# Performance work log

Measured on AMD Instinct MI355X. Metric: run time of the kernel, lower is better.

The kernel has to match this reference:

```python
import jax, jax.numpy as jnp
import numpy as np
from jax import lax

V = 100000       # vocab_size / num_words
E = 300          # embedding_size (== num_units, required by compare stage)
M = 300          # num_units / mem_dim
NC = 3           # num_classes
L = 128          # leaves per tree -> N = 2L-1 nodes
N = 2 * L - 1


def build_tree(num_leaves):
    # balanced binary tree, postorder node numbering (children before parent)
    left, right = [], []
    def rec(lo, hi):
        if hi - lo == 1:
            left.append(-1); right.append(-1)
            return len(left) - 1
        mid = (lo + hi) // 2
        l = rec(lo, mid)
        r = rec(mid, hi)
        left.append(l); right.append(r)
        return len(left) - 1
    rec(0, num_leaves)
    return np.asarray(left, np.int32), np.asarray(right, np.int32)


def setup_inputs() -> dict:
    key = jax.random.key(0)
    ks = jax.random.split(key, 20)
    l1, r1 = build_tree(L)
    l2, r2 = build_tree(L)
    s = 0.1  # param scale (stands in for orthogonal init)
    inp = {
        "sent1": jax.random.randint(ks[0], (N,), 0, V),
        "sent2": jax.random.randint(ks[1], (N,), 0, V),
        "left1": jnp.asarray(l1), "right1": jnp.asarray(r1),
        "left2": jnp.asarray(l2), "right2": jnp.asarray(r2),
        "emb": jax.random.normal(ks[2], (V, E), jnp.float32),
        # composer x-projections, gate order: [cx, ix, fx, ox]
        "Wx_i": jax.random.normal(ks[3], (4, M, E), jnp.float32) * s,
        "bx_i": jnp.zeros((4, M), jnp.float32),
        # composer h-projections, gate order: [u, i, lf, rf, o]
        "Wl_i": jax.random.normal(ks[4], (5, M, M), jnp.float32) * s,
        "Wr_i": jax.random.normal(ks[5], (5, M, M), jnp.float32) * s,
        "Wx_c": jax.random.normal(ks[6], (4, M, M), jnp.float32) * s,
        "bx_c": jnp.zeros((4, M), jnp.float32),
        "Wl_c": jax.random.normal(ks[7], (5, M, M), jnp.float32) * s,
        "Wr_c": jax.random.normal(ks[8], (5, M, M), jnp.float32) * s,
        "Wc": jax.random.normal(ks[9], (M, 4 * M), jnp.float32) * 0.01,
        "bc": jnp.zeros((M,), jnp.float32),
        "Wa1": jax.random.normal(ks[10], (M, 4 * M), jnp.float32) * 0.01,
        "ba1": jnp.zeros((M,), jnp.float32),
        "Wa2": jax.random.normal(ks[11], (NC, M), jnp.float32) * 0.01,
        "ba2": jnp.zeros((NC,), jnp.float32),
    }
    return inp


def tree_lstm(xg, left, right, Wl, Wr):
    # xg: [N, 4, M] precomputed x-gate terms (cx, ix, fx, ox)
    # Wl/Wr: [5, M, M] hidden-state gate weights (u, i, lf, rf, o)
    n, _, m = xg.shape
    zero = jnp.zeros((m,), xg.dtype)

    def step(carry, t):
        C, H = carry
        i, l, r = t
        lc = jnp.where(l >= 0, C[jnp.maximum(l, 0)], zero)
        lh = jnp.where(l >= 0, H[jnp.maximum(l, 0)], zero)
        rc = jnp.where(r >= 0, C[jnp.maximum(r, 0)], zero)
        rh = jnp.where(r >= 0, H[jnp.maximum(r, 0)], zero)
        gl = jnp.einsum('gmd,d->gm', Wl, lh)  # [5, M]
        gr = jnp.einsum('gmd,d->gm', Wr, rh)
        x = xg[i]  # [4, M]
        u  = jnp.tanh(x[0] + gl[0] + gr[0])
        ig = jax.nn.sigmoid(x[1] + gl[1] + gr[1])
        lf = jax.nn.sigmoid(x[2] + gl[2] + gr[2])  # fx shared for both forgets (as in source)
        rf = jax.nn.sigmoid(x[2] + gl[3] + gr[3])
        c = ig * u + lf * lc + rf * rc
        o = jax.nn.sigmoid(x[3] + gl[4] + gr[4])
        h = o * jnp.tanh(c)
        return (C.at[i].set(c), H.at[i].set(h)), None

    init = (jnp.zeros((n, m), xg.dtype), jnp.zeros((n, m), xg.dtype))
    (_, H), _ = lax.scan(step, init, (jnp.arange(n), left, right))
    return H  # [N, M] all node hidden states in postorder


def reference(sent1, sent2, left1, right1, left2, right2, emb,
              Wx_i, bx_i, Wl_i, Wr_i, Wx_c, bx_c, Wl_c, Wr_c,
              Wc, bc, Wa1, ba1, Wa2, ba2):
    pad = emb.shape[0] - 1  # num_words - 1

    def encode(sent, left, right):
        # leaves embed their token; internal nodes embed PAD (PAD=True path)
        tok = jnp.where(left < 0, sent, pad)
        x = emb[tok]                                        # [N, E]
        xg = jnp.einsum('nd,gmd->ngm', x, Wx_i) + bx_i      # [N, 4, M]
        return tree_lstm(xg, left, right, Wl_i, Wr_i)

    s1 = encode(sent1, left1, right1)  # [N1, M]
    s2 = encode(sent2, left2, right2)  # [N2, M]

    raw = s1 @ s2.T                                         # [N1, N2]
    beta = jax.nn.softmax(raw, axis=1) @ s2                 # aligned to s1
    alpha = jax.nn.softmax(raw.T, axis=1) @ s1              # aligned to s2

    def compare(s, a, left, right):
        feat = jnp.concatenate([s, a, s - a, s * a], axis=-1)  # [N, 4M]
        h = jax.nn.relu(feat @ Wc.T + bc)                      # [N, M]
        xg = jnp.einsum('nd,gmd->ngm', h, Wx_c) + bx_c
        return tree_lstm(xg, left, right, Wl_c, Wr_c)

    v1 = compare(s1, beta, left1, right1)
    v2 = compare(s2, alpha, left2, right2)

    agg = jnp.concatenate([v1.mean(0), v1.max(0), v2.mean(0), v2.max(0)])  # [4M]
    hidden = jax.nn.relu(agg @ Wa1.T + ba1)
    logits = hidden @ Wa2.T + ba2
    return logits[None, :]  # [1, num_classes]
```

## Files before the change

### kernel.cpp

```cpp
#include <hip/hip_runtime.h>
#include <math.h>

#define NN 255
#define MM 300
#define TC 510
#define NBLK 300
#define CHUNK 16

__device__ __forceinline__ float sigm(float x) { return 1.0f / (1.0f + expf(-x)); }

__device__ __forceinline__ float aload(const float* p) {
  return __hip_atomic_load(p, __ATOMIC_RELAXED, __HIP_MEMORY_SCOPE_AGENT);
}
__device__ __forceinline__ void astore(float* p, float v) {
  __hip_atomic_store(p, v, __ATOMIC_RELAXED, __HIP_MEMORY_SCOPE_AGENT);
}

__device__ __forceinline__ void leaf_gate(const float* __restrict__ xgp, int m, float& c, float& h) {
  float x0 = xgp[m], x1 = xgp[300 + m], x3 = xgp[900 + m];
  float u  = tanhf(x0);
  float ig = sigm(x1);
  c = ig * u;
  h = sigm(x3) * tanhf(c);
}

__device__ __forceinline__ void gsync(unsigned* flags, unsigned phase) {
  asm volatile("s_waitcnt vmcnt(0)" ::: "memory");
  __syncthreads();
  unsigned* gate = flags + NBLK;
  if (blockIdx.x == 0) {
    if (threadIdx.x < 64) {
      for (;;) {
        unsigned mn = phase;
        for (int i = 1 + (int)threadIdx.x; i < NBLK; i += 64)
          mn = min(mn, __hip_atomic_load(&flags[i], __ATOMIC_RELAXED, __HIP_MEMORY_SCOPE_AGENT));
        if (__all(mn >= phase)) break;
        __builtin_amdgcn_s_sleep(2);
      }
      if (threadIdx.x == 0)
        __hip_atomic_store(gate, phase, __ATOMIC_RELAXED, __HIP_MEMORY_SCOPE_AGENT);
    }
  } else {
    if (threadIdx.x == 0) {
      __hip_atomic_store(&flags[blockIdx.x], phase, __ATOMIC_RELAXED, __HIP_MEMORY_SCOPE_AGENT);
      while (__hip_atomic_load(gate, __ATOMIC_RELAXED, __HIP_MEMORY_SCOPE_AGENT) < phase)
        __builtin_amdgcn_s_sleep(2);
    }
  }
  __syncthreads();
}

__global__ __launch_bounds__(512) void k_setup(const int* __restrict__ l1, const int* __restrict__ r1,
                                               const int* __restrict__ l2, const int* __restrict__ r2,
                                               int* __restrict__ lists, int* __restrict__ cnt)
{
  __shared__ int lv[TC];
  __shared__ int cs[16];
  int t = threadIdx.x;
  if (t < TC) lv[t] = 0;
  if (t < 16) cs[t] = 0;
  __syncthreads();
  for (int it = 0; it < 12; ++it) {
    int nv = 0;
    if (t < TC) {
      int tr = t >= NN;
      int i  = t - tr * NN;
      const int* L = tr ? l2 : l1;
      const int* R = tr ? r2 : r1;
      int l = L[i], r = R[i];
      nv = (l < 0) ? 0 : 1 + max(lv[tr * NN + l], lv[tr * NN + r]);
    }
    __syncthreads();
    if (t < TC) lv[t] = nv;
    __syncthreads();
  }
  if (t < TC) {
    int tr = t >= NN;
    int i  = t - tr * NN;
    int v  = min(lv[t], 15);
    int pos = atomicAdd(&cs[v], 1);
    lists[v * 256 + pos] = (tr << 8) | i;
  }
  __syncthreads();
  if (t < 16) cnt[t] = cs[t];
}

__global__ __launch_bounds__(256, 2) void k_tree(
    const int* __restrict__ l1, const int* __restrict__ r1,
    const int* __restrict__ l2, const int* __restrict__ r2,
    const float* __restrict__ Wl, const float* __restrict__ Wr,
    const float* __restrict__ xg,
    float* __restrict__ H, float* __restrict__ C,
    const int* __restrict__ lists, const int* __restrict__ cnt,
    unsigned* __restrict__ bar)
{
  __shared__ float Hs[CHUNK][2][320];
  __shared__ float Cs[CHUNK][4][2];
  __shared__ float Xs[CHUNK][4][4];
  __shared__ int es[CHUNK], lcs[CHUNK], rcs[CHUNK];

  const int tid  = threadIdx.x;
  const int lane = tid & 63;
  const int team = tid >> 6;
  const int mblk = blockIdx.x % 75;
  const int grp  = blockIdx.x / 75;
  const int m    = mblk * 4 + team;

  float wl[5][5], wr[5][5];
  #pragma unroll
  for (int g = 0; g < 5; ++g) {
    #pragma unroll
    for (int j = 0; j < 5; ++j) {
      int d = j * 64 + lane;
      size_t o = ((size_t)g * 300 + m) * 300 + d;
      wl[g][j] = (d < 300) ? Wl[o] : 0.f;
      wr[g][j] = (d < 300) ? Wr[o] : 0.f;
    }
  }

  for (int e = blockIdx.x * 256 + tid; e < TC * 300; e += 256 * NBLK) {
    int gi = e / 300;
    int mm = e - gi * 300;
    int tr = gi >= NN;
    int node = gi - tr * NN;
    if ((tr ? l2 : l1)[node] < 0) {
      float c, h;
      leaf_gate(xg + (size_t)gi * 1200, mm, c, h);
      astore(&C[(size_t)gi * 300 + mm], c);
      astore(&H[(size_t)gi * 300 + mm], h);
    }
  }
  gsync(bar, 1);

  for (int lv = 1; lv <= 7; ++lv) {
    int nodes = cnt[lv];
    int npg = (nodes + 3) >> 2;
    int n0 = grp * npg;
    int n1 = min(nodes, n0 + npg);
    for (int nb = n0; nb < n1; nb += CHUNK) {
      int nch = min(CHUNK, n1 - nb);
      __syncthreads();
      if (tid < nch) {
        int e = lists[lv * 256 + nb + tid];
        int tr = e >> 8, node = e & 255;
        es[tid]  = e;
        lcs[tid] = (tr ? l2 : l1)[node];
        rcs[tid] = (tr ? r2 : r1)[node];
      }
      __syncthreads();
      for (int q = tid; q < nch * 8; q += 256) {
        int ni = q >> 3, tm = (q >> 1) & 3, side = q & 1;
        int tr = es[ni] >> 8;
        int child = side ? rcs[ni] : lcs[ni];
        Cs[ni][tm][side] = aload(&C[(size_t)(tr * NN + child) * 300 + mblk * 4 + tm]);
      }
      for (int q = tid; q < nch * 16; q += 256) {
        int ni = q >> 4, tm = (q >> 2) & 3, g = q & 3;
        int e = es[ni];
        int gi = (e >> 8) * NN + (e & 255);
        Xs[ni][tm][g] = xg[(size_t)gi * 1200 + g * 300 + mblk * 4 + tm];
      }
      for (int idx = tid; idx < nch * 640; idx += 256) {
        int ni   = idx / 640;
        int rem  = idx - ni * 640;
        int side = rem >= 320;
        int d    = rem - side * 320;
        float v = 0.f;
        if (d < 300) {
          int tr    = es[ni] >> 8;
          int child = side ? rcs[ni] : lcs[ni];
          v = aload(&H[(size_t)(tr * NN + child) * 300 + d]);
        }
        Hs[ni][side][d] = v;
      }
      __syncthreads();
      #pragma unroll 2
      for (int ni = 0; ni < nch; ++ni) {
        float p0 = 0.f, p1 = 0.f, p2 = 0.f, p3 = 0.f, p4 = 0.f;
        #pragma unroll
        for (int j = 0; j < 5; ++j) {
          float hl = Hs[ni][0][j * 64 + lane];
          float hr = Hs[ni][1][j * 64 + lane];
          p0 += wl[0][j] * hl + wr[0][j] * hr;
          p1 += wl[1][j] * hl + wr[1][j] * hr;
          p2 += wl[2][j] * hl + wr[2][j] * hr;
          p3 += wl[3][j] * hl + wr[3][j] * hr;
          p4 += wl[4][j] * hl + wr[4][j] * hr;
        }
        #pragma unroll
        for (int off = 32; off; off >>= 1) {
          p0 += __shfl_xor(p0, off);
          p1 += __shfl_xor(p1, off);
          p2 += __shfl_xor(p2, off);
          p3 += __shfl_xor(p3, off);
          p4 += __shfl_xor(p4, off);
        }
        if (lane == 0) {
          int e = es[ni];
          int gi = (e >> 8) * NN + (e & 255);
          float lc = Cs[ni][team][0], rc = Cs[ni][team][1];
          float u  = tanhf(Xs[ni][team][0] + p0);
          float ig = sigm (Xs[ni][team][1] + p1);
          float lf = sigm (Xs[ni][team][2] + p2);
          float rf = sigm (Xs[ni][team][2] + p3);
          float o  = sigm (Xs[ni][team][3] + p4);
          float cc = ig * u + lf * lc + rf * rc;
          astore(&C[(size_t)gi * 300 + m], cc);
          astore(&H[(size_t)gi * 300 + m], o * tanhf(cc));
        }
      }
    }
    if (lv < 7) gsync(bar, 1 + lv);
  }
}

__global__ __launch_bounds__(256) void k_xg(const int* __restrict__ sent1, const int* __restrict__ sent2,
                                            const int* __restrict__ l1, const int* __restrict__ l2,
                                            const float* __restrict__ emb, int pad,
                                            const float* __restrict__ W, const float* __restrict__ bias,
                                            const float* __restrict__ hsrc, float* __restrict__ out)
{
  __shared__ float Z[8][300];
  int tx = threadIdx.x, ty = threadIdx.y;
  int t = ty * 64 + tx;
  int colbase = blockIdx.y * 8;
  for (int c = 0; c < 8; ++c) {
    int gcol = colbase + c;
    if (gcol < TC) {
      if (hsrc) {
        for (int k = t; k < 300; k += 256) Z[c][k] = hsrc[(size_t)gcol * 300 + k];
      } else {
        int tr = gcol >= NN;
        int node = gcol - tr * NN;
        const int* L = tr ? l2 : l1;
        const int* S = tr ? sent2 : sent1;
        int tok = (L[node] < 0) ? S[node] : pad;
        const float* e = emb + (size_t)tok * 300;
        for (int k = t; k < 300; k += 256) Z[c][k] = e[k];
      }
    } else {
      for (int k = t; k < 300; k += 256) Z[c][k] = 0.f;
    }
  }
  __syncthreads();
  int r = blockIdx.x * 64 + tx;
  if (r < 1200) {
    float a0 = 0.f, a1 = 0.f;
    const float* wp = W + (size_t)r * 300;
    for (int k = 0; k < 300; k += 4) {
      float4 wv = *(const float4*)(wp + k);
      float4 z0 = *(const float4*)(&Z[ty][k]);
      float4 z1 = *(const float4*)(&Z[ty + 4][k]);
      a0 += wv.x*z0.x + wv.y*z0.y + wv.z*z0.z + wv.w*z0.w;
      a1 += wv.x*z1.x + wv.y*z1.y + wv.z*z1.z + wv.w*z1.w;
    }
    float b = bias[r];
    int g0 = colbase + ty, g1 = colbase + ty + 4;
    if (g0 < TC) out[(size_t)g0 * 1200 + r] = a0 + b;
    if (g1 < TC) out[(size_t)g1 * 1200 + r] = a1 + b;
  }
}

__global__ __launch_bounds__(256) void k_attn(const float* __restrict__ Henc, float* __restrict__ ab)
{
  __shared__ float q[300];
  __shared__ float pr[NN];
  __shared__ float red[256];
  int b = blockIdx.x, t = threadIdx.x;
  int dir = b >= NN;
  int i = b - dir * NN;
  const float* Ss = Henc + (dir ? NN * 300 : 0);
  const float* So = Henc + (dir ? 0 : NN * 300);
  for (int k = t; k < 300; k += 256) q[k] = Ss[(size_t)i * 300 + k];
  __syncthreads();
  float v = -1e30f;
  if (t < NN) {
    const float* row = So + (size_t)t * 300;
    float a = 0.f;
    for (int k = 0; k < 300; k += 4) {
      float4 rv = *(const float4*)(row + k);
      float4 qv = *(const float4*)(&q[k]);
      a += rv.x*qv.x + rv.y*qv.y + rv.z*qv.z + rv.w*qv.w;
    }
    pr[t] = a;
    v = a;
  }
  red[t] = v;
  __syncthreads();
  for (int s = 128; s > 0; s >>= 1) { if (t < s) red[t] = fmaxf(red[t], red[t + s]); __syncthreads(); }
  float mx = red[0];
  __syncthreads();
  float e = 0.f;
  if (t < NN) { e = expf(pr[t] - mx); pr[t] = e; }
  red[t] = e;
  __syncthreads();
  for (int s = 128; s > 0; s >>= 1) { if (t < s) red[t] += red[t + s]; __syncthreads(); }
  float inv = 1.0f / red[0];
  __syncthreads();
  for (int m = t; m < 300; m += 256) {
    float a = 0.f;
    for (int j = 0; j < NN; ++j) a += pr[j] * So[(size_t)j * 300 + m];
    ab[(size_t)b * 300 + m] = a * inv;
  }
}

__global__ __launch_bounds__(256) void k_hcmp(const float* __restrict__ Henc, const float* __restrict__ ab,
                                              const float* __restrict__ Wc, const float* __restrict__ bc,
                                              float* __restrict__ hc)
{
  __shared__ float Z[8][1200];
  int tx = threadIdx.x, ty = threadIdx.y;
  int t = ty * 64 + tx;
  int colbase = blockIdx.y * 8;
  for (int c = 0; c < 8; ++c) {
    int gcol = colbase + c;
    if (gcol < TC) {
      const float* sp = Henc + (size_t)gcol * 300;
      const float* ap = ab + (size_t)gcol * 300;
      for (int k = t; k < 1200; k += 256) {
        int sel = k >= 900 ? 3 : (k >= 600 ? 2 : (k >= 300 ? 1 : 0));
        int kk = k - sel * 300;
        float s = sp[kk], a = ap[kk];
        Z[c][k] = sel == 0 ? s : sel == 1 ? a : sel == 2 ? (s - a) : (s * a);
      }
    } else {
      for (int k = t; k < 1200; k += 256) Z[c][k] = 0.f;
    }
  }
  __syncthreads();
  int r = blockIdx.x * 64 + tx;
  if (r < 300) {
    float a0 = 0.f, a1 = 0.f;
    const float* wp = Wc + (size_t)r * 1200;
    for (int k = 0; k < 1200; k += 4) {
      float4 wv = *(const float4*)(wp + k);
      float4 z0 = *(const float4*)(&Z[ty][k]);
      float4 z1 = *(const float4*)(&Z[ty + 4][k]);
      a0 += wv.x*z0.x + wv.y*z0.y + wv.z*z0.z + wv.w*z0.w;
      a1 += wv.x*z1.x + wv.y*z1.y + wv.z*z1.z + wv.w*z1.w;
    }
    float b = bc[r];
    int g0 = colbase + ty, g1 = colbase + ty + 4;
    if (g0 < TC) hc[(size_t)g0 * 300 + r] = fmaxf(a0 + b, 0.f);
    if (g1 < TC) hc[(size_t)g1 * 300 + r] = fmaxf(a1 + b, 0.f);
  }
}

__global__ __launch_bounds__(256) void k_agg(const float* __restrict__ Hcmp, float* __restrict__ agg)
{
  int tr = blockIdx.x, t = threadIdx.x;
  for (int m = t; m < 300; m += 256) {
    float s = 0.f, mx = -1e30f;
    const float* hp = Hcmp + (size_t)tr * NN * 300 + m;
    for (int n = 0; n < NN; ++n) { float v = hp[(size_t)n * 300]; s += v; mx = fmaxf(mx, v); }
    agg[tr * 600 + m] = s / 255.0f;
    agg[tr * 600 + 300 + m] = mx;
  }
}

__global__ __launch_bounds__(512) void k_mlp(const float* __restrict__ agg,
                                             const float* __restrict__ Wa1, const float* __restrict__ ba1,
                                             const float* __restrict__ Wa2, const float* __restrict__ ba2,
                                             float* __restrict__ out)
{
  __shared__ float a_s[1200];
  __shared__ float hid[300];
  int t = threadIdx.x;
  for (int k = t; k < 1200; k += 512) a_s[k] = agg[k];
  __syncthreads();
  for (int h = t; h < 300; h += 512) {
    float acc = ba1[h];
    const float* wp = Wa1 + (size_t)h * 1200;
    for (int k = 0; k < 1200; k += 4) {
      float4 wv = *(const float4*)(wp + k);
      float4 av = *(const float4*)(&a_s[k]);
      acc += wv.x*av.x + wv.y*av.y + wv.z*av.z + wv.w*av.w;
    }
    hid[h] = fmaxf(acc, 0.f);
  }
  __syncthreads();
  if (t < 192) {
    int c = t >> 6, lane = t & 63;
    float a = 0.f;
    for (int k = lane; k < 300; k += 64) a += Wa2[c * 300 + k] * hid[k];
    for (int off = 32; off > 0; off >>= 1) a += __shfl_down(a, off);
    if (lane == 0) out[c] = a + ba2[c];
  }
}

extern "C" void kernel_launch(void* const* d_in, const int* in_sizes, int n_in,
                              void* d_out, int out_size, void* d_ws, size_t ws_size,
                              hipStream_t stream)
{
  const int*   sent1 = (const int*)d_in[0];
  const int*   sent2 = (const int*)d_in[1];
  const int*   l1    = (const int*)d_in[2];
  const int*   r1    = (const int*)d_in[3];
  const int*   l2    = (const int*)d_in[4];
  const int*   r2    = (const int*)d_in[5];
  const float* emb   = (const float*)d_in[6];
  const float* Wx_i  = (const float*)d_in[7];
  const float* bx_i  = (const float*)d_in[8];
  const float* Wl_i  = (const float*)d_in[9];
  const float* Wr_i  = (const float*)d_in[10];
  const float* Wx_c  = (const float*)d_in[11];
  const float* bx_c  = (const float*)d_in[12];
  const float* Wl_c  = (const float*)d_in[13];
  const float* Wr_c  = (const float*)d_in[14];
  const float* Wc    = (const float*)d_in[15];
  const float* bc    = (const float*)d_in[16];
  const float* Wa1   = (const float*)d_in[17];
  const float* ba1   = (const float*)d_in[18];
  const float* Wa2   = (const float*)d_in[19];
  const float* ba2   = (const float*)d_in[20];
  int V = in_sizes[6] / 300;
  int pad = V - 1;

  char* w = (char*)d_ws;
  unsigned* bar1 = (unsigned*)w;
  unsigned* bar2 = (unsigned*)(w + 2048);
  int* cnt   = (int*)(w + 4096);
  int* lists = (int*)(w + 4160);
  float* xg   = (float*)(w + 20544);
  float* Henc = xg + 612000;
  float* Hcmp = Henc + 153000;
  float* C    = Hcmp + 153000;
  float* ab   = C + 153000;
  float* hc   = ab + 153000;
  float* agg  = hc + 153000;

  hipMemsetAsync((void*)bar1, 0, 4096, stream);
  k_setup<<<1, 512, 0, stream>>>(l1, r1, l2, r2, lists, cnt);

  dim3 blk(64, 4);

  k_xg<<<dim3(19, 64), blk, 0, stream>>>(sent1, sent2, l1, l2, emb, pad, Wx_i, bx_i, nullptr, xg);
  {
    void* args[] = {(void*)&l1, (void*)&r1, (void*)&l2, (void*)&r2,
                    (void*)&Wl_i, (void*)&Wr_i, (void*)&xg,
                    (void*)&Henc, (void*)&C, (void*)&lists, (void*)&cnt, (void*)&bar1};
    hipLaunchCooperativeKernel((void*)k_tree, dim3(NBLK), dim3(256), args, 0, stream);
  }

  k_attn<<<TC, 256, 0, stream>>>(Henc, ab);

  k_hcmp<<<dim3(5, 64), blk, 0, stream>>>(Henc, ab, Wc, bc, hc);
  k_xg<<<dim3(19, 64), blk, 0, stream>>>(sent1, sent2, l1, l2, emb, pad, Wx_c, bx_c, hc, xg);
  {
    void* args[] = {(void*)&l1, (void*)&r1, (void*)&l2, (void*)&r2,
                    (void*)&Wl_c, (void*)&Wr_c, (void*)&xg,
                    (void*)&Hcmp, (void*)&C, (void*)&lists, (void*)&cnt, (void*)&bar2};
    hipLaunchCooperativeKernel((void*)k_tree, dim3(NBLK), dim3(256), args, 0, stream);
  }

  k_agg<<<2, 256, 0, stream>>>(Hcmp, agg);
  k_mlp<<<1, 512, 0, stream>>>(agg, Wa1, ba1, Wa2, ba2, (float*)d_out);
}
```

Before: 550.7 us.

## Precompute child-index lists, write transposed H, fuse agg into head kernel

The setup kernel now stores each node's global index and both child indices as an int4, and the tree kernel caches these lists in shared memory once. This removes per-chunk lookups into the left/right arrays. The tree kernel also writes a transposed copy of H so the attention dot products and the mean/max aggregation read coalesced columns, and the aggregation is folded into the MLP head to drop one launch. Child H rows are gathered with explicit unrolled per-team loads. The cost is extra scattered transposed stores on the serial critical path, plus more registers in the cooperative kernel.

```diff
diff --git a/kernel.cpp b/kernel.cpp
--- a/kernel.cpp
+++ b/kernel.cpp
@@ -6,6 +6,7 @@
 #define TC 510
 #define NBLK 300
 #define CHUNK 16
+#define HTLD 512
 
 __device__ __forceinline__ float sigm(float x) { return 1.0f / (1.0f + expf(-x)); }
 
@@ -52,7 +53,7 @@
 
 __global__ __launch_bounds__(512) void k_setup(const int* __restrict__ l1, const int* __restrict__ r1,
                                                const int* __restrict__ l2, const int* __restrict__ r2,
-                                               int* __restrict__ lists, int* __restrict__ cnt)
+                                               int4* __restrict__ lists2, int* __restrict__ cnt)
 {
   __shared__ int lv[TC];
   __shared__ int cs[16];
@@ -79,25 +80,26 @@
     int i  = t - tr * NN;
     int v  = min(lv[t], 15);
     int pos = atomicAdd(&cs[v], 1);
-    lists[v * 256 + pos] = (tr << 8) | i;
+    int l = (tr ? l2 : l1)[i], r = (tr ? r2 : r1)[i];
+    lists2[v * 256 + pos] = make_int4(tr * NN + i, tr * NN + max(l, 0), tr * NN + max(r, 0), 0);
   }
   __syncthreads();
   if (t < 16) cnt[t] = cs[t];
 }
 
 __global__ __launch_bounds__(256, 2) void k_tree(
-    const int* __restrict__ l1, const int* __restrict__ r1,
-    const int* __restrict__ l2, const int* __restrict__ r2,
+    const int* __restrict__ l1, const int* __restrict__ l2,
     const float* __restrict__ Wl, const float* __restrict__ Wr,
     const float* __restrict__ xg,
-    float* __restrict__ H, float* __restrict__ C,
-    const int* __restrict__ lists, const int* __restrict__ cnt,
+    float* __restrict__ H, float* __restrict__ C, float* __restrict__ HT,
+    const int4* __restrict__ lists2, const int* __restrict__ cnt,
     unsigned* __restrict__ bar)
 {
   __shared__ float Hs[CHUNK][2][320];
   __shared__ float Cs[CHUNK][4][2];
   __shared__ float Xs[CHUNK][4][4];
-  __shared__ int es[CHUNK], lcs[CHUNK], rcs[CHUNK];
+  __shared__ int4 nfo[288];
+  __shared__ int lvoff[9];
 
   const int tid  = threadIdx.x;
   const int lane = tid & 63;
@@ -117,6 +119,12 @@
       wr[g][j] = (d < 300) ? Wr[o] : 0.f;
     }
   }
+
+  if (tid == 0) { int o = 0; for (int lv = 1; lv <= 7; ++lv) { lvoff[lv] = o; o += cnt[lv]; } }
+  __syncthreads();
+  for (int lv = 1; lv <= 7; ++lv)
+    for (int i = tid; i < cnt[lv]; i += 256)
+      nfo[lvoff[lv] + i] = lists2[lv * 256 + i];
 
   for (int e = blockIdx.x * 256 + tid; e < TC * 300; e += 256 * NBLK) {
     int gi = e / 300;
@@ -128,6 +136,7 @@
       leaf_gate(xg + (size_t)gi * 1200, mm, c, h);
       astore(&C[(size_t)gi * 300 + mm], c);
       astore(&H[(size_t)gi * 300 + mm], h);
+      astore(&HT[(size_t)mm * HTLD + gi], h);
     }
   }
   gsync(bar, 1);
@@ -139,41 +148,62 @@
     int n1 = min(nodes, n0 + npg);
     for (int nb = n0; nb < n1; nb += CHUNK) {
       int nch = min(CHUNK, n1 - nb);
+      int base = lvoff[lv] + nb;
       __syncthreads();
-      if (tid < nch) {
-        int e = lists[lv * 256 + nb + tid];
-        int tr = e >> 8, node = e & 255;
-        es[tid]  = e;
-        lcs[tid] = (tr ? l2 : l1)[node];
-        rcs[tid] = (tr ? r2 : r1)[node];
+
+      #pragma unroll
+      for (int p = 0; p < 2; ++p) {
+        int niA = team + p * 8;
+        int niB = niA + 4;
+        bool vA = niA < nch, vB = niB < nch;
+        int4 na = vA ? nfo[base + niA] : make_int4(0, 0, 0, 0);
+        int4 nb4 = vB ? nfo[base + niB] : make_int4(0, 0, 0, 0);
+        float bA0, bA1, bA2, bA3, bA4, bA5, bA6, bA7, bA8, bA9;
+        float bB0, bB1, bB2, bB3, bB4, bB5, bB6, bB7, bB8, bB9;
+        #define LD(side_ptr, d, ok) ((ok) ? aload(&H[(size_t)(side_ptr) * 300 + (d)]) : 0.f)
+        {
+          int d0 = lane, d1 = 64 + lane, d2 = 128 + lane, d3 = 192 + lane, d4 = 256 + lane;
+          bool i4 = d4 < 300;
+          bA0 = LD(na.y, d0, vA); bA1 = LD(na.y, d1, vA); bA2 = LD(na.y, d2, vA);
+          bA3 = LD(na.y, d3, vA); bA4 = LD(na.y, d4, vA && i4);
+          bA5 = LD(na.z, d0, vA); bA6 = LD(na.z, d1, vA); bA7 = LD(na.z, d2, vA);
+          bA8 = LD(na.z, d3, vA); bA9 = LD(na.z, d4, vA && i4);
+          bB0 = LD(nb4.y, d0, vB); bB1 = LD(nb4.y, d1, vB); bB2 = LD(nb4.y, d2, vB);
+          bB3 = LD(nb4.y, d3, vB); bB4 = LD(nb4.y, d4, vB && i4);
+          bB5 = LD(nb4.z, d0, vB); bB6 = LD(nb4.z, d1, vB); bB7 = LD(nb4.z, d2, vB);
+          bB8 = LD(nb4.z, d3, vB); bB9 = LD(nb4.z, d4, vB && i4);
+          if (vA) {
+            Hs[niA][0][d0] = bA0; Hs[niA][0][d1] = bA1; Hs[niA][0][d2] = bA2;
+            Hs[niA][0][d3] = bA3; Hs[niA][0][d4] = bA4;
+            Hs[niA][1][d0] = bA5; Hs[niA][1][d1] = bA6; Hs[niA][1][d2] = bA7;
+            Hs[niA][1][d3] = bA8; Hs[niA][1][d4] = bA9;
+          }
+          if (vB) {
+            Hs[niB][0][d0] = bB0; Hs[niB][0][d1] = bB1; Hs[niB][0][d2] = bB2;
+            Hs[niB][0][d3] = bB3; Hs[niB][0][d4] = bB4;
+            Hs[niB][1][d0] = bB5; Hs[niB][1][d1] = bB6; Hs[niB][1][d2] = bB7;
+            Hs[niB][1][d3] = bB8; Hs[niB][1][d4] = bB9;
+          }
+        }
+        #undef LD
+      }
+      if (tid < 128) {
+        int ni = tid >> 3, tm = (tid >> 1) & 3, side = tid & 1;
+        if (ni < nch) {
+          int4 nn = nfo[base + ni];
+          int child = side ? nn.z : nn.y;
+          Cs[ni][tm][side] = aload(&C[(size_t)child * 300 + mblk * 4 + tm]);
+        }
+      }
+      {
+        int ni = tid >> 4, tm = (tid >> 2) & 3, g = tid & 3;
+        if (ni < nch) {
+          int4 nn = nfo[base + ni];
+          Xs[ni][tm][g] = xg[(size_t)nn.x * 1200 + g * 300 + mblk * 4 + tm];
+        }
       }
       __syncthreads();
-      for (int q = tid; q < nch * 8; q += 256) {
-        int ni = q >> 3, tm = (q >> 1) & 3, side = q & 1;
-        int tr = es[ni] >> 8;
-        int child = side ? rcs[ni] : lcs[ni];
-        Cs[ni][tm][side] = aload(&C[(size_t)(tr * NN + child) * 300 + mblk * 4 + tm]);
-      }
-      for (int q = tid; q < nch * 16; q += 256) {
-        int ni = q >> 4, tm = (q >> 2) & 3, g = q & 3;
-        int e = es[ni];
-        int gi = (e >> 8) * NN + (e & 255);
-        Xs[ni][tm][g] = xg[(size_t)gi * 1200 + g * 300 + mblk * 4 + tm];
-      }
-      for (int idx = tid; idx < nch * 640; idx += 256) {
-        int ni   = idx / 640;
-        int rem  = idx - ni * 640;
-        int side = rem >= 320;
-        int d    = rem - side * 320;
-        float v = 0.f;
-        if (d < 300) {
-          int tr    = es[ni] >> 8;
-          int child = side ? rcs[ni] : lcs[ni];
-          v = aload(&H[(size_t)(tr * NN + child) * 300 + d]);
-        }
-        Hs[ni][side][d] = v;
-      }
-      __syncthreads();
+
       #pragma unroll 2
       for (int ni = 0; ni < nch; ++ni) {
         float p0 = 0.f, p1 = 0.f, p2 = 0.f, p3 = 0.f, p4 = 0.f;
@@ -196,8 +226,8 @@
           p4 += __shfl_xor(p4, off);
         }
         if (lane == 0) {
-          int e = es[ni];
-          int gi = (e >> 8) * NN + (e & 255);
+          int4 nn = nfo[base + ni];
+          int gi = nn.x;
           float lc = Cs[ni][team][0], rc = Cs[ni][team][1];
           float u  = tanhf(Xs[ni][team][0] + p0);
           float ig = sigm (Xs[ni][team][1] + p1);
@@ -205,8 +235,10 @@
           float rf = sigm (Xs[ni][team][2] + p3);
           float o  = sigm (Xs[ni][team][3] + p4);
           float cc = ig * u + lf * lc + rf * rc;
+          float hv = o * tanhf(cc);
           astore(&C[(size_t)gi * 300 + m], cc);
-          astore(&H[(size_t)gi * 300 + m], o * tanhf(cc));
+          astore(&H[(size_t)gi * 300 + m], hv);
+          astore(&HT[(size_t)m * HTLD + gi], hv);
         }
       }
     }
@@ -261,7 +293,8 @@
   }
 }
 
-__global__ __launch_bounds__(256) void k_attn(const float* __restrict__ Henc, float* __restrict__ ab)
+__global__ __launch_bounds__(256) void k_attn(const float* __restrict__ H, const float* __restrict__ HT,
+                                              float* __restrict__ ab)
 {
   __shared__ float q[300];
   __shared__ float pr[NN];
@@ -269,19 +302,17 @@
   int b = blockIdx.x, t = threadIdx.x;
   int dir = b >= NN;
   int i = b - dir * NN;
-  const float* Ss = Henc + (dir ? NN * 300 : 0);
-  const float* So = Henc + (dir ? 0 : NN * 300);
+  const float* Ss = H + (dir ? NN * 300 : 0);
+  const float* So = H + (dir ? 0 : NN * 300);
+  int oppb = dir ? 0 : NN;
   for (int k = t; k < 300; k += 256) q[k] = Ss[(size_t)i * 300 + k];
   __syncthreads();
   float v = -1e30f;
   if (t < NN) {
-    const float* row = So + (size_t)t * 300;
     float a = 0.f;
-    for (int k = 0; k < 300; k += 4) {
-      float4 rv = *(const float4*)(row + k);
-      float4 qv = *(const float4*)(&q[k]);
-      a += rv.x*qv.x + rv.y*qv.y + rv.z*qv.z + rv.w*qv.w;
-    }
+    const float* hp = HT + oppb + t;
+    #pragma unroll 4
+    for (int k = 0; k < 300; ++k) a += q[k] * hp[(size_t)k * HTLD];
     pr[t] = a;
     v = a;
   }
@@ -346,27 +377,23 @@
   }
 }
 
-__global__ __launch_bounds__(256) void k_agg(const float* __restrict__ Hcmp, float* __restrict__ agg)
-{
-  int tr = blockIdx.x, t = threadIdx.x;
-  for (int m = t; m < 300; m += 256) {
-    float s = 0.f, mx = -1e30f;
-    const float* hp = Hcmp + (size_t)tr * NN * 300 + m;
-    for (int n = 0; n < NN; ++n) { float v = hp[(size_t)n * 300]; s += v; mx = fmaxf(mx, v); }
-    agg[tr * 600 + m] = s / 255.0f;
-    agg[tr * 600 + 300 + m] = mx;
-  }
-}
-
-__global__ __launch_bounds__(512) void k_mlp(const float* __restrict__ agg,
-                                             const float* __restrict__ Wa1, const float* __restrict__ ba1,
-                                             const float* __restrict__ Wa2, const float* __restrict__ ba2,
-                                             float* __restrict__ out)
+__global__ __launch_bounds__(512) void k_head(const float* __restrict__ HTc,
+                                              const float* __restrict__ Wa1, const float* __restrict__ ba1,
+                                              const float* __restrict__ Wa2, const float* __restrict__ ba2,
+                                              float* __restrict__ out)
 {
   __shared__ float a_s[1200];
   __shared__ float hid[300];
   int t = threadIdx.x;
-  for (int k = t; k < 1200; k += 512) a_s[k] = agg[k];
+  for (int idx = t; idx < 600; idx += 512) {
+    int tr = idx >= 300;
+    int m = idx - tr * 300;
+    const float* p = HTc + (size_t)m * HTLD + tr * NN;
+    float s = 0.f, mx = -1e30f;
+    for (int n = 0; n < NN; ++n) { float v = p[n]; s += v; mx = fmaxf(mx, v); }
+    a_s[tr * 600 + m] = s / 255.0f;
+    a_s[tr * 600 + 300 + m] = mx;
+  }
   __syncthreads();
   for (int h = t; h < 300; h += 512) {
     float acc = ba1[h];
@@ -419,40 +446,42 @@
   char* w = (char*)d_ws;
   unsigned* bar1 = (unsigned*)w;
   unsigned* bar2 = (unsigned*)(w + 2048);
-  int* cnt   = (int*)(w + 4096);
-  int* lists = (int*)(w + 4160);
-  float* xg   = (float*)(w + 20544);
+  int* cnt     = (int*)(w + 4096);
+  int4* lists2 = (int4*)(w + 4160);
+  float* xg   = (float*)(w + 4160 + 65536);
   float* Henc = xg + 612000;
   float* Hcmp = Henc + 153000;
   float* C    = Hcmp + 153000;
   float* ab   = C + 153000;
   float* hc   = ab + 153000;
-  float* agg  = hc + 153000;
+  float* HTe  = hc + 153000;
+  float* HTc  = HTe + 153600;
 
   hipMemsetAsync((void*)bar1, 0, 4096, stream);
-  k_setup<<<1, 512, 0, stream>>>(l1, r1, l2, r2, lists, cnt);
+  k_setup<<<1, 512, 0, stream>>>(l1, r1, l2, r2, lists2, cnt);
 
   dim3 blk(64, 4);
 
   k_xg<<<dim3(19, 64), blk, 0, stream>>>(sent1, sent2, l1, l2, emb, pad, Wx_i, bx_i, nullptr, xg);
   {
-    void* args[] = {(void*)&l1, (void*)&r1, (void*)&l2, (void*)&r2,
+    void* args[] = {(void*)&l1, (void*)&l2,
                     (void*)&Wl_i, (void*)&Wr_i, (void*)&xg,
-                    (void*)&Henc, (void*)&C, (void*)&lists, (void*)&cnt, (void*)&bar1};
+                    (void*)&Henc, (void*)&C, (void*)&HTe,
+                    (void*)&lists2, (void*)&cnt, (void*)&bar1};
     hipLaunchCooperativeKernel((void*)k_tree, dim3(NBLK), dim3(256), args, 0, stream);
   }
 
-  k_attn<<<TC, 256, 0, stream>>>(Henc, ab);
+  k_attn<<<TC, 256, 0, stream>>>(Henc, HTe, ab);
 
   k_hcmp<<<dim3(5, 64), blk, 0, stream>>>(Henc, ab, Wc, bc, hc);
   k_xg<<<dim3(19, 64), blk, 0, stream>>>(sent1, sent2, l1, l2, emb, pad, Wx_c, bx_c, hc, xg);
   {
-    void* args[] = {(void*)&l1, (void*)&r1, (void*)&l2, (void*)&r2,
+    void* args[] = {(void*)&l1, (void*)&l2,
                     (void*)&Wl_c, (void*)&Wr_c, (void*)&xg,
-                    (void*)&Hcmp, (void*)&C, (void*)&lists, (void*)&cnt, (void*)&bar2};
+                    (void*)&Hcmp, (void*)&C, (void*)&HTc,
+                    (void*)&lists2, (void*)&cnt, (void*)&bar2};
     hipLaunchCooperativeKernel((void*)k_tree, dim3(NBLK), dim3(256), args, 0, stream);
   }
 
-  k_agg<<<2, 256, 0, stream>>>(Hcmp, agg);
-  k_mlp<<<1, 512, 0, stream>>>(agg, Wa1, ba1, Wa2, ba2, (float*)d_out);
-}
+  k_head<<<1, 512, 0, stream>>>(HTc, Wa1, ba1, Wa2, ba2, (float*)d_out);
+}
```

Result: faster. 503.8 us (-8.5%).
